# Optimization experiments

Measured on AMD Instinct MI355X. Metric: run time of the kernel, lower is better.

Reference implementation:

```python
import jax, jax.numpy as jnp
import numpy as np

# Residue-type multiplicative bonuses from _add_chemical_property_bonuses
# dict: {1:1.3, 3:1.2, 6:1.2, 8:1.4, 11:1.3, 13:1.5, 17:1.6, 18:1.4, 19:1.1,
#        0:1.05, 2:1.1, 5:1.1, 15:1.05, 16:1.05}, default 1.0
_BOND_TABLE = np.full(20, 1.0, dtype=np.float32)
for k, v in {1: 1.3, 3: 1.2, 6: 1.2, 8: 1.4, 11: 1.3, 13: 1.5, 17: 1.6,
             18: 1.4, 19: 1.1, 0: 1.05, 2: 1.1, 5: 1.1, 15: 1.05, 16: 1.05}.items():
    _BOND_TABLE[k] = v

DIRECT_R = 3.5    # direct contact radius (A)
EXT_R = 8.0       # extended interaction radius (A)
NEIGH_R2 = 25.0   # surface-accessibility neighbor radius squared (5 A)^2


def setup_inputs() -> dict:
    key = jax.random.key(0)
    k1, k2, k3, k4 = jax.random.split(key, 4)
    N, M, F = 16384, 64, 16
    pos = jax.random.uniform(k1, (N, 3), dtype=jnp.float32) * 40.0          # protein box
    ligand_pos = jax.random.uniform(k2, (M, 3), dtype=jnp.float32) * 10.0 + 15.0  # centered ligand
    x = jax.random.normal(k3, (N, F), dtype=jnp.float32)
    res = jax.random.randint(k4, (N,), 0, 20)
    x = x.at[:, 1].set(res.astype(jnp.float32))  # column 1 = residue type code
    return {"pos": pos, "ligand_pos": ligand_pos, "x": x, "max_atoms": 512}


def reference(pos, ligand_pos, x, max_atoms):
    # --- min distance of each pocket atom to any ligand atom: [N]
    d2l_sq = jnp.sum((pos[:, None, :] - ligand_pos[None, :, :]) ** 2, axis=-1)  # [N, M]
    min_d = jnp.sqrt(jnp.maximum(jnp.min(d2l_sq, axis=1), 1e-12))               # [N]

    direct = min_d <= DIRECT_R
    extended = (min_d > DIRECT_R) & (min_d <= EXT_R)
    far = min_d > EXT_R

    # --- surface accessibility among far atoms only (as in torch: pos[far_mask])
    # Compare squared distances (equivalent to d<5 & d>0, avoids sqrt on the NxN block).
    sq = jnp.sum((pos[:, None, :] - pos[None, :, :]) ** 2, axis=-1)  # [N, N]
    neigh = (sq < NEIGH_R2) & (sq > 0.0) & far[None, :]              # neighbors within far subset
    counts = jnp.where(far, jnp.sum(neigh, axis=1).astype(pos.dtype), 0.0)
    max_n = jnp.max(counts)
    max_n = jnp.where(max_n > 0, max_n, 1.0)
    surface = 1.0 - counts / (max_n + 1e-6)

    # --- tiered scores
    scores = jnp.where(
        direct, 10.0,
        jnp.where(extended, 5.0 * (EXT_R - min_d) / EXT_R, surface))

    # --- chemical property bonuses (vectorized lookup-table gather)
    res_type = jnp.clip(x[:, 1].astype(jnp.int32), 0, 19)
    scores = scores * jnp.asarray(_BOND_TABLE)[res_type]

    top_scores, indices = jax.lax.top_k(scores, max_atoms)
    return scores, top_scores, indices
```

## Files before the change

### kernel.cpp

```cpp
#include <hip/hip_runtime.h>
#include <stdint.h>

#define NCELLS 512
#define NHIST 2048
#define SCAP 2560
#define CCAP 4096

__device__ __constant__ float BOND[20] = {
    1.05f, 1.30f, 1.10f, 1.20f, 1.00f, 1.10f, 1.20f, 1.00f, 1.40f, 1.00f,
    1.00f, 1.30f, 1.00f, 1.50f, 1.00f, 1.05f, 1.05f, 1.60f, 1.40f, 1.10f};

__device__ __forceinline__ int clamp8(int v) { return v < 0 ? 0 : (v > 7 ? 7 : v); }

__global__ void k_classify(const float* __restrict__ pos, const float* __restrict__ lig,
                           float* __restrict__ minD, int N, int M) {
#pragma clang fp contract(off)
  __shared__ float sl[768];
  int t = threadIdx.x;
  for (int idx = t; idx < 3 * M; idx += blockDim.x) sl[idx] = lig[idx];
  __syncthreads();
  int i = blockIdx.x * blockDim.x + t;
  if (i >= N) return;
  float px = pos[3 * i], py = pos[3 * i + 1], pz = pos[3 * i + 2];
  float m = 3.4e38f;
  for (int j = 0; j < M; ++j) {
    float dx = px - sl[3 * j];
    float dy = py - sl[3 * j + 1];
    float dz = pz - sl[3 * j + 2];
    float d2 = dx * dx + dy * dy + dz * dz;
    m = fminf(m, d2);
  }
  minD[i] = sqrtf(fmaxf(m, 1e-12f));
}

__global__ void __launch_bounds__(1024) k_build(const float* __restrict__ pos,
                                                const float* __restrict__ minD,
                                                int* __restrict__ cellStart,
                                                float4* __restrict__ sortedPos,
                                                int* __restrict__ hist,
                                                int* __restrict__ scalars, int N) {
#pragma clang fp contract(off)
  __shared__ int lh[NCELLS];
  __shared__ int s[NCELLS];
  __shared__ int lcur[NCELLS];
  int t = threadIdx.x;
  if (t < NCELLS) lh[t] = 0;
  hist[t] = 0;
  hist[t + 1024] = 0;
  if (t < 4) scalars[t] = 0;
  __syncthreads();
  for (int i = t; i < N; i += 1024) {
    if (minD[i] > 8.0f) {
      int cx = clamp8((int)(pos[3 * i] * 0.2f));
      int cy = clamp8((int)(pos[3 * i + 1] * 0.2f));
      int cz = clamp8((int)(pos[3 * i + 2] * 0.2f));
      atomicAdd(&lh[(cz * 8 + cy) * 8 + cx], 1);
    }
  }
  __syncthreads();
  if (t < NCELLS) s[t] = lh[t];
  __syncthreads();
  for (int off = 1; off < NCELLS; off <<= 1) {
    int v = (t < NCELLS && t >= off) ? s[t - off] : 0;
    __syncthreads();
    if (t < NCELLS) s[t] += v;
    __syncthreads();
  }
  if (t < NCELLS) {
    int e = s[t] - lh[t];
    cellStart[t] = e;
    lcur[t] = e;
  }
  if (t == NCELLS - 1) cellStart[NCELLS] = s[t];
  __syncthreads();
  for (int i = t; i < N; i += 1024) {
    if (minD[i] > 8.0f) {
      float px = pos[3 * i], py = pos[3 * i + 1], pz = pos[3 * i + 2];
      int cx = clamp8((int)(px * 0.2f));
      int cy = clamp8((int)(py * 0.2f));
      int cz = clamp8((int)(pz * 0.2f));
      int slot = atomicAdd(&lcur[(cz * 8 + cy) * 8 + cx], 1);
      sortedPos[slot] = make_float4(px, py, pz, __int_as_float(i));
    }
  }
}

__global__ void __launch_bounds__(256) k_query(const float4* __restrict__ sortedPos,
                                               const int* __restrict__ cellStart,
                                               int* __restrict__ counts,
                                               int* __restrict__ scalars) {
#pragma clang fp contract(off)
  __shared__ float4 sa[SCAP];
  int c = blockIdx.x;
  int t = threadIdx.x;
  int qs = cellStart[c], qe = cellStart[c + 1];
  int nc = qe - qs;
  if (nc == 0) return;
  int cx = c & 7, cy = (c >> 3) & 7, cz = c >> 6;
  int x0 = cx > 0 ? cx - 1 : 0, x1 = cx < 7 ? cx + 1 : 7;
  int y0 = cy > 0 ? cy - 1 : 0, y1 = cy < 7 ? cy + 1 : 7;
  int z0 = cz > 0 ? cz - 1 : 0, z1 = cz < 7 ? cz + 1 : 7;
  int S = 0;
  for (int z = z0; z <= z1; ++z) {
    for (int y = y0; y <= y1; ++y) {
      int rb = (z * 8 + y) * 8;
      int k0 = cellStart[rb + x0];
      int k1 = cellStart[rb + x1 + 1];
      int len = k1 - k0;
      if (len > SCAP - S) len = SCAP - S;
      for (int k = t; k < len; k += 256) sa[S + k] = sortedPos[k0 + k];
      if (len > 0) S += len;
    }
  }
  __syncthreads();
  int wave = t >> 6, lane = t & 63;
  int wmax = 0;
  for (int a = wave; a < nc; a += 4) {
    float4 qp = sortedPos[qs + a];
    int cnt = 0;
    for (int u = lane; u < S; u += 64) {
      float4 p = sa[u];
      float dx = qp.x - p.x;
      float dy = qp.y - p.y;
      float dz = qp.z - p.z;
      float d2 = dx * dx + dy * dy + dz * dz;
      cnt += (d2 < 25.0f && d2 > 0.0f) ? 1 : 0;
    }
    cnt += __shfl_xor(cnt, 1, 64);
    cnt += __shfl_xor(cnt, 2, 64);
    cnt += __shfl_xor(cnt, 4, 64);
    cnt += __shfl_xor(cnt, 8, 64);
    cnt += __shfl_xor(cnt, 16, 64);
    cnt += __shfl_xor(cnt, 32, 64);
    if (lane == 0) counts[__float_as_int(qp.w)] = cnt;
    wmax = wmax > cnt ? wmax : cnt;
  }
  if (lane == 0 && wmax > 0) atomicMax(&scalars[0], wmax);
}

__global__ void k_score(const float* __restrict__ minD, const int* __restrict__ counts,
                        const int* __restrict__ scalars, const float* __restrict__ x,
                        float* __restrict__ out_scores, uint64_t* __restrict__ keys,
                        int* __restrict__ hist, int N, int F) {
#pragma clang fp contract(off)
  __shared__ int lh[NHIST];
  for (int b = threadIdx.x; b < NHIST; b += blockDim.x) lh[b] = 0;
  __syncthreads();
  int i = blockIdx.x * blockDim.x + threadIdx.x;
  if (i < N) {
    float md = minD[i];
    float mn = (float)scalars[0];
    if (!(mn > 0.0f)) mn = 1.0f;
    float score;
    if (md <= 3.5f) {
      score = 10.0f;
    } else if (md <= 8.0f) {
      score = 5.0f * (8.0f - md) / 8.0f;
    } else {
      float cf = (float)counts[i];
      score = 1.0f - cf / (mn + 1e-6f);
    }
    int rt = (int)x[(size_t)i * F + 1];
    rt = rt < 0 ? 0 : (rt > 19 ? 19 : rt);
    score = score * BOND[rt];
    out_scores[i] = score;
    uint32_t fb = __float_as_uint(score);
    keys[i] = ((uint64_t)fb << 32) | (uint64_t)(0x7FFFFFFFu - (uint32_t)i);
    atomicAdd(&lh[fb >> 20], 1);
  }
  __syncthreads();
  for (int b = threadIdx.x; b < NHIST; b += blockDim.x) {
    int v = lh[b];
    if (v) atomicAdd(&hist[b], v);
  }
}

__global__ void __launch_bounds__(1024) k_select(const uint64_t* __restrict__ keys,
                                                 const int* __restrict__ hist,
                                                 float* __restrict__ out_top,
                                                 float* __restrict__ out_idx,
                                                 int N, int K) {
  __shared__ int s[1024];
  __shared__ int bShared;
  __shared__ int candCnt;
  __shared__ uint64_t cand[CCAP];
  int t = threadIdx.x;
  int l0 = hist[2 * t], l1 = hist[2 * t + 1];
  s[t] = l0 + l1;
  if (t == 0) candCnt = 0;
  __syncthreads();
  for (int off = 1; off < 1024; off <<= 1) {
    int v = (t + off < 1024) ? s[t + off] : 0;
    __syncthreads();
    s[t] += v;
    __syncthreads();
  }
  int cumNext = (t < 1023) ? s[t + 1] : 0;
  if (s[t] >= K && cumNext < K) {
    bShared = (cumNext + l1 >= K) ? (2 * t + 1) : (2 * t);
  }
  __syncthreads();
  int B = bShared;
  for (int i = t; i < N; i += 1024) {
    uint64_t k = keys[i];
    if ((int)(k >> 52) >= B) {
      int p = atomicAdd(&candCnt, 1);
      if (p < CCAP) cand[p] = k;
    }
  }
  __syncthreads();
  int C = candCnt;
  if (C > CCAP) C = CCAP;
  for (int j = t; j < C; j += 1024) {
    uint64_t kj = cand[j];
    int r = 0;
    for (int u = 0; u < C; ++u) r += (cand[u] > kj) ? 1 : 0;
    if (r < K) {
      out_top[r] = __uint_as_float((uint32_t)(kj >> 32));
      out_idx[r] = (float)(0x7FFFFFFFu - (uint32_t)kj);
    }
  }
}

extern "C" void kernel_launch(void* const* d_in, const int* in_sizes, int n_in,
                              void* d_out, int out_size, void* d_ws, size_t ws_size,
                              hipStream_t stream) {
  const float* pos = (const float*)d_in[0];
  const float* lig = (const float*)d_in[1];
  const float* x   = (const float*)d_in[2];
  int N = in_sizes[0] / 3;
  int M = in_sizes[1] / 3;
  int F = in_sizes[2] / N;
  int K = (out_size - N) / 2;

  char* ws = (char*)d_ws;
  size_t off = 0;
  float4*   sortedPos = (float4*)(ws + off);   off += (size_t)N * 16;
  uint64_t* keys      = (uint64_t*)(ws + off); off += (size_t)N * 8;
  float*    minD      = (float*)(ws + off);    off += (size_t)N * 4;
  int*      counts    = (int*)(ws + off);      off += (size_t)N * 4;
  int*      cellStart = (int*)(ws + off);      off += (size_t)(NCELLS + 1) * 4;
  int*      hist      = (int*)(ws + off);      off += (size_t)NHIST * 4;
  int*      scalars   = (int*)(ws + off);      off += 16;

  float* out_scores = (float*)d_out;
  float* out_top    = out_scores + N;
  float* out_idx    = out_top + K;

  int nb = (N + 255) / 256;

  hipLaunchKernelGGL(k_classify, dim3(nb),     dim3(256),  0, stream, pos, lig, minD, N, M);
  hipLaunchKernelGGL(k_build,    dim3(1),      dim3(1024), 0, stream, pos, minD, cellStart, sortedPos, hist, scalars, N);
  hipLaunchKernelGGL(k_query,    dim3(NCELLS), dim3(256),  0, stream, sortedPos, cellStart, counts, scalars);
  hipLaunchKernelGGL(k_score,    dim3(nb),     dim3(256),  0, stream, minD, counts, scalars, x, out_scores, keys, hist, N, F);
  hipLaunchKernelGGL(k_select,   dim3(1),      dim3(1024), 0, stream, keys, hist, out_top, out_idx, N, K);
}
```

Baseline: 142.8 us.

## Fuse all stages into one cooperative persistent kernel with grid syncs

```diff
diff --git a/kernel.cpp b/kernel.cpp
--- a/kernel.cpp
+++ b/kernel.cpp
@@ -1,10 +1,15 @@
 #include <hip/hip_runtime.h>
+#include <hip/hip_cooperative_groups.h>
 #include <stdint.h>
+
+namespace cg = cooperative_groups;
 
 #define NCELLS 512
 #define NHIST 2048
 #define SCAP 2560
 #define CCAP 4096
+#define GRIDB 512
+#define BLKT 256
 
 __device__ __constant__ float BOND[20] = {
     1.05f, 1.30f, 1.10f, 1.20f, 1.00f, 1.10f, 1.20f, 1.00f, 1.40f, 1.00f,
@@ -12,142 +17,136 @@
 
 __device__ __forceinline__ int clamp8(int v) { return v < 0 ? 0 : (v > 7 ? 7 : v); }
 
-__global__ void k_classify(const float* __restrict__ pos, const float* __restrict__ lig,
-                           float* __restrict__ minD, int N, int M) {
+__global__ void __launch_bounds__(BLKT) k_fused(
+    const float* __restrict__ pos, const float* __restrict__ lig,
+    const float* __restrict__ x,
+    float* __restrict__ out_scores, float* __restrict__ out_top,
+    float* __restrict__ out_idx,
+    float4* __restrict__ sortedPos, uint64_t* __restrict__ keys,
+    float* __restrict__ minD, int* __restrict__ counts,
+    int* __restrict__ cellStart, int* __restrict__ cellCount,
+    int* __restrict__ cellCursor, int* __restrict__ hist,
+    int* __restrict__ scalars, int N, int M, int F, int K) {
 #pragma clang fp contract(off)
-  __shared__ float sl[768];
+  cg::grid_group grid = cg::this_grid();
+  __shared__ char smem[SCAP * 16];
   int t = threadIdx.x;
-  for (int idx = t; idx < 3 * M; idx += blockDim.x) sl[idx] = lig[idx];
+  int b = blockIdx.x;
+  int gid = b * BLKT + t;
+  int gsz = GRIDB * BLKT;
+
+  float* sl = (float*)smem;
+  for (int idx = t; idx < 3 * M; idx += BLKT) sl[idx] = lig[idx];
+
+  for (int i = gid; i < NCELLS; i += gsz) cellCount[i] = 0;
+  for (int i = gid; i < NHIST; i += gsz) hist[i] = 0;
+  if (gid < 4) scalars[gid] = 0;
   __syncthreads();
-  int i = blockIdx.x * blockDim.x + t;
-  if (i >= N) return;
-  float px = pos[3 * i], py = pos[3 * i + 1], pz = pos[3 * i + 2];
-  float m = 3.4e38f;
-  for (int j = 0; j < M; ++j) {
-    float dx = px - sl[3 * j];
-    float dy = py - sl[3 * j + 1];
-    float dz = pz - sl[3 * j + 2];
-    float d2 = dx * dx + dy * dy + dz * dz;
-    m = fminf(m, d2);
-  }
-  minD[i] = sqrtf(fmaxf(m, 1e-12f));
-}
-
-__global__ void __launch_bounds__(1024) k_build(const float* __restrict__ pos,
-                                                const float* __restrict__ minD,
-                                                int* __restrict__ cellStart,
-                                                float4* __restrict__ sortedPos,
-                                                int* __restrict__ hist,
-                                                int* __restrict__ scalars, int N) {
-#pragma clang fp contract(off)
-  __shared__ int lh[NCELLS];
-  __shared__ int s[NCELLS];
-  __shared__ int lcur[NCELLS];
-  int t = threadIdx.x;
-  if (t < NCELLS) lh[t] = 0;
-  hist[t] = 0;
-  hist[t + 1024] = 0;
-  if (t < 4) scalars[t] = 0;
-  __syncthreads();
-  for (int i = t; i < N; i += 1024) {
-    if (minD[i] > 8.0f) {
-      int cx = clamp8((int)(pos[3 * i] * 0.2f));
-      int cy = clamp8((int)(pos[3 * i + 1] * 0.2f));
-      int cz = clamp8((int)(pos[3 * i + 2] * 0.2f));
-      atomicAdd(&lh[(cz * 8 + cy) * 8 + cx], 1);
-    }
-  }
-  __syncthreads();
-  if (t < NCELLS) s[t] = lh[t];
-  __syncthreads();
-  for (int off = 1; off < NCELLS; off <<= 1) {
-    int v = (t < NCELLS && t >= off) ? s[t - off] : 0;
+  grid.sync();
+
+  for (int i = gid; i < N; i += gsz) {
+    float px = pos[3 * i], py = pos[3 * i + 1], pz = pos[3 * i + 2];
+    float m = 3.4e38f;
+    for (int j = 0; j < M; ++j) {
+      float dx = px - sl[3 * j];
+      float dy = py - sl[3 * j + 1];
+      float dz = pz - sl[3 * j + 2];
+      float d2 = dx * dx + dy * dy + dz * dz;
+      m = fminf(m, d2);
+    }
+    float md = sqrtf(fmaxf(m, 1e-12f));
+    minD[i] = md;
+    if (md > 8.0f) {
+      int cx = clamp8((int)(px * 0.2f));
+      int cy = clamp8((int)(py * 0.2f));
+      int cz = clamp8((int)(pz * 0.2f));
+      atomicAdd(&cellCount[(cz * 8 + cy) * 8 + cx], 1);
+    }
+  }
+  grid.sync();
+
+  if (b == 0) {
+    int* s = (int*)smem;
+    int c0 = cellCount[2 * t], c1 = cellCount[2 * t + 1];
+    int p = c0 + c1;
+    s[t] = p;
     __syncthreads();
-    if (t < NCELLS) s[t] += v;
-    __syncthreads();
-  }
-  if (t < NCELLS) {
-    int e = s[t] - lh[t];
-    cellStart[t] = e;
-    lcur[t] = e;
-  }
-  if (t == NCELLS - 1) cellStart[NCELLS] = s[t];
-  __syncthreads();
-  for (int i = t; i < N; i += 1024) {
+    for (int off = 1; off < 256; off <<= 1) {
+      int v = (t >= off) ? s[t - off] : 0;
+      __syncthreads();
+      s[t] += v;
+      __syncthreads();
+    }
+    int excl = s[t] - p;
+    cellStart[2 * t] = excl;          cellCursor[2 * t] = excl;
+    cellStart[2 * t + 1] = excl + c0; cellCursor[2 * t + 1] = excl + c0;
+    if (t == 255) cellStart[NCELLS] = s[255];
+  }
+  grid.sync();
+
+  for (int i = gid; i < N; i += gsz) {
     if (minD[i] > 8.0f) {
       float px = pos[3 * i], py = pos[3 * i + 1], pz = pos[3 * i + 2];
       int cx = clamp8((int)(px * 0.2f));
       int cy = clamp8((int)(py * 0.2f));
       int cz = clamp8((int)(pz * 0.2f));
-      int slot = atomicAdd(&lcur[(cz * 8 + cy) * 8 + cx], 1);
+      int slot = atomicAdd(&cellCursor[(cz * 8 + cy) * 8 + cx], 1);
       sortedPos[slot] = make_float4(px, py, pz, __int_as_float(i));
     }
   }
-}
-
-__global__ void __launch_bounds__(256) k_query(const float4* __restrict__ sortedPos,
-                                               const int* __restrict__ cellStart,
-                                               int* __restrict__ counts,
-                                               int* __restrict__ scalars) {
-#pragma clang fp contract(off)
-  __shared__ float4 sa[SCAP];
-  int c = blockIdx.x;
-  int t = threadIdx.x;
-  int qs = cellStart[c], qe = cellStart[c + 1];
-  int nc = qe - qs;
-  if (nc == 0) return;
-  int cx = c & 7, cy = (c >> 3) & 7, cz = c >> 6;
-  int x0 = cx > 0 ? cx - 1 : 0, x1 = cx < 7 ? cx + 1 : 7;
-  int y0 = cy > 0 ? cy - 1 : 0, y1 = cy < 7 ? cy + 1 : 7;
-  int z0 = cz > 0 ? cz - 1 : 0, z1 = cz < 7 ? cz + 1 : 7;
-  int S = 0;
-  for (int z = z0; z <= z1; ++z) {
-    for (int y = y0; y <= y1; ++y) {
-      int rb = (z * 8 + y) * 8;
-      int k0 = cellStart[rb + x0];
-      int k1 = cellStart[rb + x1 + 1];
-      int len = k1 - k0;
-      if (len > SCAP - S) len = SCAP - S;
-      for (int k = t; k < len; k += 256) sa[S + k] = sortedPos[k0 + k];
-      if (len > 0) S += len;
-    }
-  }
-  __syncthreads();
-  int wave = t >> 6, lane = t & 63;
-  int wmax = 0;
-  for (int a = wave; a < nc; a += 4) {
-    float4 qp = sortedPos[qs + a];
-    int cnt = 0;
-    for (int u = lane; u < S; u += 64) {
-      float4 p = sa[u];
-      float dx = qp.x - p.x;
-      float dy = qp.y - p.y;
-      float dz = qp.z - p.z;
-      float d2 = dx * dx + dy * dy + dz * dz;
-      cnt += (d2 < 25.0f && d2 > 0.0f) ? 1 : 0;
-    }
-    cnt += __shfl_xor(cnt, 1, 64);
-    cnt += __shfl_xor(cnt, 2, 64);
-    cnt += __shfl_xor(cnt, 4, 64);
-    cnt += __shfl_xor(cnt, 8, 64);
-    cnt += __shfl_xor(cnt, 16, 64);
-    cnt += __shfl_xor(cnt, 32, 64);
-    if (lane == 0) counts[__float_as_int(qp.w)] = cnt;
-    wmax = wmax > cnt ? wmax : cnt;
-  }
-  if (lane == 0 && wmax > 0) atomicMax(&scalars[0], wmax);
-}
-
-__global__ void k_score(const float* __restrict__ minD, const int* __restrict__ counts,
-                        const int* __restrict__ scalars, const float* __restrict__ x,
-                        float* __restrict__ out_scores, uint64_t* __restrict__ keys,
-                        int* __restrict__ hist, int N, int F) {
-#pragma clang fp contract(off)
-  __shared__ int lh[NHIST];
-  for (int b = threadIdx.x; b < NHIST; b += blockDim.x) lh[b] = 0;
-  __syncthreads();
-  int i = blockIdx.x * blockDim.x + threadIdx.x;
-  if (i < N) {
+  grid.sync();
+
+  {
+    int c = b;
+    int qs = cellStart[c], qe = cellStart[c + 1];
+    int nc = qe - qs;
+    if (nc > 0) {
+      float4* sa = (float4*)smem;
+      int cx = c & 7, cy = (c >> 3) & 7, cz = c >> 6;
+      int x0 = cx > 0 ? cx - 1 : 0, x1 = cx < 7 ? cx + 1 : 7;
+      int y0 = cy > 0 ? cy - 1 : 0, y1 = cy < 7 ? cy + 1 : 7;
+      int z0 = cz > 0 ? cz - 1 : 0, z1 = cz < 7 ? cz + 1 : 7;
+      int S = 0;
+      for (int z = z0; z <= z1; ++z) {
+        for (int y = y0; y <= y1; ++y) {
+          int rb = (z * 8 + y) * 8;
+          int k0 = cellStart[rb + x0];
+          int k1 = cellStart[rb + x1 + 1];
+          int len = k1 - k0;
+          if (len > SCAP - S) len = SCAP - S;
+          for (int k = t; k < len; k += BLKT) sa[S + k] = sortedPos[k0 + k];
+          if (len > 0) S += len;
+        }
+      }
+      __syncthreads();
+      int wave = t >> 6, lane = t & 63;
+      int wmax = 0;
+      for (int a = wave; a < nc; a += 4) {
+        float4 qp = sortedPos[qs + a];
+        int cnt = 0;
+        for (int u = lane; u < S; u += 64) {
+          float4 p = sa[u];
+          float dx = qp.x - p.x;
+          float dy = qp.y - p.y;
+          float dz = qp.z - p.z;
+          float d2 = dx * dx + dy * dy + dz * dz;
+          cnt += (d2 < 25.0f && d2 > 0.0f) ? 1 : 0;
+        }
+        cnt += __shfl_xor(cnt, 1, 64);
+        cnt += __shfl_xor(cnt, 2, 64);
+        cnt += __shfl_xor(cnt, 4, 64);
+        cnt += __shfl_xor(cnt, 8, 64);
+        cnt += __shfl_xor(cnt, 16, 64);
+        cnt += __shfl_xor(cnt, 32, 64);
+        if (lane == 0) counts[__float_as_int(qp.w)] = cnt;
+        wmax = wmax > cnt ? wmax : cnt;
+      }
+      if (lane == 0 && wmax > 0) atomicMax(&scalars[0], wmax);
+    }
+  }
+  grid.sync();
+
+  for (int i = gid; i < N; i += gsz) {
     float md = minD[i];
     float mn = (float)scalars[0];
     if (!(mn > 0.0f)) mn = 1.0f;
@@ -166,58 +165,64 @@
     out_scores[i] = score;
     uint32_t fb = __float_as_uint(score);
     keys[i] = ((uint64_t)fb << 32) | (uint64_t)(0x7FFFFFFFu - (uint32_t)i);
-    atomicAdd(&lh[fb >> 20], 1);
-  }
-  __syncthreads();
-  for (int b = threadIdx.x; b < NHIST; b += blockDim.x) {
-    int v = lh[b];
-    if (v) atomicAdd(&hist[b], v);
-  }
-}
-
-__global__ void __launch_bounds__(1024) k_select(const uint64_t* __restrict__ keys,
-                                                 const int* __restrict__ hist,
-                                                 float* __restrict__ out_top,
-                                                 float* __restrict__ out_idx,
-                                                 int N, int K) {
-  __shared__ int s[1024];
-  __shared__ int bShared;
-  __shared__ int candCnt;
-  __shared__ uint64_t cand[CCAP];
-  int t = threadIdx.x;
-  int l0 = hist[2 * t], l1 = hist[2 * t + 1];
-  s[t] = l0 + l1;
-  if (t == 0) candCnt = 0;
-  __syncthreads();
-  for (int off = 1; off < 1024; off <<= 1) {
-    int v = (t + off < 1024) ? s[t + off] : 0;
+    atomicAdd(&hist[fb >> 20], 1);
+  }
+  grid.sync();
+
+  if (b == 0) {
+    int* s = (int*)smem;
+    int base = t * 8;
+    int local = 0;
+    for (int q = 0; q < 8; ++q) local += hist[base + q];
+    s[t] = local;
     __syncthreads();
-    s[t] += v;
+    for (int off = 1; off < 256; off <<= 1) {
+      int v = (t + off < 256) ? s[t + off] : 0;
+      __syncthreads();
+      s[t] += v;
+      __syncthreads();
+    }
+    int cumNext = (t < 255) ? s[t + 1] : 0;
+    if (s[t] >= K && cumNext < K) {
+      int running = cumNext;
+      int B2 = base;
+      for (int q = base + 7; q >= base; --q) {
+        running += hist[q];
+        if (running >= K) { B2 = q; break; }
+      }
+      scalars[2] = B2;
+    }
+  }
+  grid.sync();
+
+  {
+    uint64_t* candG = (uint64_t*)sortedPos;
+    int B2 = scalars[2];
+    for (int i = gid; i < N; i += gsz) {
+      uint64_t k = keys[i];
+      if ((int)(k >> 52) >= B2) {
+        int p = atomicAdd(&scalars[1], 1);
+        if (p < CCAP) candG[p] = k;
+      }
+    }
+  }
+  grid.sync();
+
+  if (b < 16) {
+    uint64_t* candG = (uint64_t*)sortedPos;
+    uint64_t* sc = (uint64_t*)smem;
+    int C = scalars[1];
+    if (C > CCAP) C = CCAP;
+    for (int j = t; j < C; j += BLKT) sc[j] = candG[j];
     __syncthreads();
-  }
-  int cumNext = (t < 1023) ? s[t + 1] : 0;
-  if (s[t] >= K && cumNext < K) {
-    bShared = (cumNext + l1 >= K) ? (2 * t + 1) : (2 * t);
-  }
-  __syncthreads();
-  int B = bShared;
-  for (int i = t; i < N; i += 1024) {
-    uint64_t k = keys[i];
-    if ((int)(k >> 52) >= B) {
-      int p = atomicAdd(&candCnt, 1);
-      if (p < CCAP) cand[p] = k;
-    }
-  }
-  __syncthreads();
-  int C = candCnt;
-  if (C > CCAP) C = CCAP;
-  for (int j = t; j < C; j += 1024) {
-    uint64_t kj = cand[j];
-    int r = 0;
-    for (int u = 0; u < C; ++u) r += (cand[u] > kj) ? 1 : 0;
-    if (r < K) {
-      out_top[r] = __uint_as_float((uint32_t)(kj >> 32));
-      out_idx[r] = (float)(0x7FFFFFFFu - (uint32_t)kj);
+    for (int j = b * BLKT + t; j < C; j += 16 * BLKT) {
+      uint64_t kj = sc[j];
+      int r = 0;
+      for (int u = 0; u < C; ++u) r += (sc[u] > kj) ? 1 : 0;
+      if (r < K) {
+        out_top[r] = __uint_as_float((uint32_t)(kj >> 32));
+        out_idx[r] = (float)(0x7FFFFFFFu - (uint32_t)kj);
+      }
     }
   }
 }
@@ -240,6 +245,8 @@
   float*    minD      = (float*)(ws + off);    off += (size_t)N * 4;
   int*      counts    = (int*)(ws + off);      off += (size_t)N * 4;
   int*      cellStart = (int*)(ws + off);      off += (size_t)(NCELLS + 1) * 4;
+  int*      cellCount = (int*)(ws + off);      off += (size_t)NCELLS * 4;
+  int*      cellCursor= (int*)(ws + off);      off += (size_t)NCELLS * 4;
   int*      hist      = (int*)(ws + off);      off += (size_t)NHIST * 4;
   int*      scalars   = (int*)(ws + off);      off += 16;
 
@@ -247,11 +254,10 @@
   float* out_top    = out_scores + N;
   float* out_idx    = out_top + K;
 
-  int nb = (N + 255) / 256;
-
-  hipLaunchKernelGGL(k_classify, dim3(nb),     dim3(256),  0, stream, pos, lig, minD, N, M);
-  hipLaunchKernelGGL(k_build,    dim3(1),      dim3(1024), 0, stream, pos, minD, cellStart, sortedPos, hist, scalars, N);
-  hipLaunchKernelGGL(k_query,    dim3(NCELLS), dim3(256),  0, stream, sortedPos, cellStart, counts, scalars);
-  hipLaunchKernelGGL(k_score,    dim3(nb),     dim3(256),  0, stream, minD, counts, scalars, x, out_scores, keys, hist, N, F);
-  hipLaunchKernelGGL(k_select,   dim3(1),      dim3(1024), 0, stream, keys, hist, out_top, out_idx, N, K);
+  void* args[] = {&pos, &lig, &x, &out_scores, &out_top, &out_idx,
+                  &sortedPos, &keys, &minD, &counts,
+                  &cellStart, &cellCount, &cellCursor, &hist, &scalars,
+                  &N, &M, &F, &K};
+  hipLaunchCooperativeKernel((void*)k_fused, dim3(GRIDB), dim3(BLKT),
+                             args, 0, stream);
 }
```

Result: slower. 514.3 us (+260.2%).
